# Kernel optimization log

Measured on AMD Instinct MI355X. Metric: run time of the kernel, lower is better.

The kernel has to match this reference:

```python
import jax, jax.numpy as jnp
import numpy as np

DIM = 768
N_HEADS = 12
HEAD_DIM = DIM // N_HEADS
BATCH = 2
SEQ = 4096


def setup_inputs() -> dict:
    key = jax.random.key(0)
    ks = jax.random.split(key, 9)
    s = 1.0 / np.sqrt(DIM)
    return {
        "x": jax.random.normal(ks[0], (BATCH, SEQ, DIM), dtype=jnp.float32),
        "Wq": jax.random.normal(ks[1], (DIM, DIM), dtype=jnp.float32) * s,
        "bq": jax.random.normal(ks[2], (DIM,), dtype=jnp.float32) * s,
        "Wk": jax.random.normal(ks[3], (DIM, DIM), dtype=jnp.float32) * s,
        "bk": jax.random.normal(ks[4], (DIM,), dtype=jnp.float32) * s,
        "Wv": jax.random.normal(ks[5], (DIM, DIM), dtype=jnp.float32) * s,
        "bv": jax.random.normal(ks[6], (DIM,), dtype=jnp.float32) * s,
        "Wo": jax.random.normal(ks[7], (DIM, DIM), dtype=jnp.float32) * s,
        "bo": jax.random.normal(ks[8], (DIM,), dtype=jnp.float32) * s,
    }


def reference(x, Wq, bq, Wk, bk, Wv, bv, Wo, bo):
    B, S, D = x.shape
    scale = 1.0 / np.sqrt(HEAD_DIM).astype(np.float32)
    # projections: [B,S,D] -> [B,H,S,Hd]
    def split_heads(t):
        return t.reshape(B, S, N_HEADS, HEAD_DIM).transpose(0, 2, 1, 3)
    q = split_heads(x @ Wq + bq)
    k = split_heads(x @ Wk + bk)
    v = split_heads(x @ Wv + bv)
    # full score matrix [B,H,S,S] as in the original (memory-bound)
    scores = jnp.einsum("bhqd,bhkd->bhqk", q, k) * scale
    attn = jax.nn.softmax(scores, axis=-1)
    out = jnp.einsum("bhqk,bhkd->bhqd", attn, v)
    out = out.transpose(0, 2, 1, 3).reshape(B, S, D)
    return out @ Wo + bo
```

## Files before the change

### kernel.cpp

```cpp
#include <hip/hip_runtime.h>
#include <hip/hip_bf16.h>
#include <math.h>

#define D_MODEL 768
#define NH 12
#define HD 64
#define BATCH 2
#define SEQ 4096
#define NROWS (BATCH * SEQ)

#define QSCALE 0.18033688011112042f

typedef __attribute__((ext_vector_type(8))) short short8;
typedef __attribute__((ext_vector_type(4))) short short4v;
typedef __attribute__((ext_vector_type(4))) float f32x4;
typedef __attribute__((ext_vector_type(16))) float f32x16;
typedef __attribute__((ext_vector_type(4))) unsigned int uint4v;

__device__ inline unsigned short f2bf(float f) {
    __hip_bfloat16 h = __float2bfloat16(f);
    return *reinterpret_cast<unsigned short*>(&h);
}

__device__ __forceinline__ unsigned int cvtpk_bf16(float lo, float hi) {
    unsigned int d;
    asm("v_cvt_pk_bf16_f32 %0, %1, %2" : "=v"(d) : "v"(lo), "v"(hi));
    return d;
}

__device__ __forceinline__ short8 u4_as_s8(uint4v u) {
    return *reinterpret_cast<short8*>(&u);
}

__device__ __forceinline__ void async_ld16(const unsigned short* g, unsigned short* l) {
    __builtin_amdgcn_global_load_lds(
        (const __attribute__((address_space(1))) void*)g,
        (__attribute__((address_space(3))) void*)l, 16, 0, 0);
}

__global__ __launch_bounds__(256) void convert_x_k(
    const float* __restrict__ x, unsigned short* __restrict__ xb)
{
    size_t i = ((size_t)blockIdx.x * 256 + threadIdx.x) * 8;
    float4 a = *(const float4*)(x + i);
    float4 b = *(const float4*)(x + i + 4);
    short8 o;
    o[0] = (short)f2bf(a.x); o[1] = (short)f2bf(a.y);
    o[2] = (short)f2bf(a.z); o[3] = (short)f2bf(a.w);
    o[4] = (short)f2bf(b.x); o[5] = (short)f2bf(b.y);
    o[6] = (short)f2bf(b.z); o[7] = (short)f2bf(b.w);
    *(short8*)(xb + i) = o;
}

__global__ __launch_bounds__(256) void convert_wt_k(
    const float* __restrict__ Wq, const float* __restrict__ Wk,
    const float* __restrict__ Wv, const float* __restrict__ Wo,
    unsigned short* __restrict__ wt)
{
    const float* W = (blockIdx.z == 0) ? Wq : (blockIdx.z == 1) ? Wk
                   : (blockIdx.z == 2) ? Wv : Wo;
    unsigned short* dst = wt + (size_t)blockIdx.z * D_MODEL * D_MODEL;
    __shared__ float tile[64][65];
    const int k0 = blockIdx.x * 64, n0 = blockIdx.y * 64;
    const int t = threadIdx.x;
    const int r = t >> 2, seg = t & 3;
    const float* src = W + (size_t)(k0 + r) * D_MODEL + n0 + seg * 16;
    #pragma unroll
    for (int i = 0; i < 4; ++i) {
        float4 v = *(const float4*)(src + i * 4);
        tile[r][seg * 16 + i * 4 + 0] = v.x;
        tile[r][seg * 16 + i * 4 + 1] = v.y;
        tile[r][seg * 16 + i * 4 + 2] = v.z;
        tile[r][seg * 16 + i * 4 + 3] = v.w;
    }
    __syncthreads();
    unsigned short* d = dst + (size_t)(n0 + r) * D_MODEL + k0 + seg * 16;
    short8 o0, o1;
    #pragma unroll
    for (int j = 0; j < 8; ++j) o0[j] = (short)f2bf(tile[seg * 16 + j][r]);
    #pragma unroll
    for (int j = 0; j < 8; ++j) o1[j] = (short)f2bf(tile[seg * 16 + 8 + j][r]);
    *(short8*)(d) = o0;
    *(short8*)(d + 8) = o1;
}

__global__ __launch_bounds__(256, 3) void qkv_fused_k(
    const unsigned short* __restrict__ xb,
    const unsigned short* __restrict__ wt,
    const float* __restrict__ bq, const float* __restrict__ bk,
    const float* __restrict__ bv,
    unsigned short* __restrict__ qb,
    unsigned short* __restrict__ kb,
    unsigned short* __restrict__ vtb)
{
    __shared__ unsigned short As[128][64];
    __shared__ unsigned short Bs[3][64][64];
    const int t = threadIdx.x;
    const int w = t >> 6, lane = t & 63, quad = lane >> 4, col = lane & 15;
    const int r0 = blockIdx.x * 128;
    const int c0 = blockIdx.y * 64;

    f32x4 acc[3][2][4] = {};

    for (int kk = 0; kk < D_MODEL; kk += 64) {
        __syncthreads();
        #pragma unroll
        for (int j = 0; j < 4; ++j) {
            int c = (w * 4 + j) * 64 + lane;
            async_ld16(xb + (size_t)(r0 + (c >> 3)) * D_MODEL + kk + (c & 7) * 8,
                       &As[0][0] + (size_t)c * 8);
        }
        #pragma unroll
        for (int z = 0; z < 3; ++z) {
            const unsigned short* Wt = wt + (size_t)z * D_MODEL * D_MODEL;
            #pragma unroll
            for (int j = 0; j < 2; ++j) {
                int c = (w * 2 + j) * 64 + lane;
                async_ld16(Wt + (size_t)(c0 + (c >> 3)) * D_MODEL + kk + (c & 7) * 8,
                           &Bs[z][0][0] + (size_t)c * 8);
            }
        }
        __syncthreads();
        #pragma unroll
        for (int ks = 0; ks < 2; ++ks) {
            short8 af[2];
            af[0] = *(const short8*)&As[w * 32 + col][ks * 32 + quad * 8];
            af[1] = *(const short8*)&As[w * 32 + 16 + col][ks * 32 + quad * 8];
            #pragma unroll
            for (int z = 0; z < 3; ++z) {
                short8 bf[4];
                #pragma unroll
                for (int nt = 0; nt < 4; ++nt)
                    bf[nt] = *(const short8*)&Bs[z][nt * 16 + col][ks * 32 + quad * 8];
                #pragma unroll
                for (int mt = 0; mt < 2; ++mt)
                    #pragma unroll
                    for (int nt = 0; nt < 4; ++nt)
                        acc[z][mt][nt] = __builtin_amdgcn_mfma_f32_16x16x32_bf16(
                            af[mt], bf[nt], acc[z][mt][nt], 0, 0, 0);
            }
        }
    }

    const int h = blockIdx.y;
    #pragma unroll
    for (int z = 0; z < 3; ++z) {
        const float* bias = (z == 0) ? bq : (z == 1) ? bk : bv;
        #pragma unroll
        for (int nt = 0; nt < 4; ++nt) {
            const float bv_ = bias[c0 + nt * 16 + col];
            const int hd = nt * 16 + col;
            #pragma unroll
            for (int mt = 0; mt < 2; ++mt) {
                #pragma unroll
                for (int reg = 0; reg < 4; ++reg) {
                    int r = r0 + w * 32 + mt * 16 + quad * 4 + reg;
                    int b = r >> 12, s = r & (SEQ - 1);
                    float val = acc[z][mt][nt][reg] + bv_;
                    size_t bh = (size_t)(b * NH + h);
                    size_t bhb = bh * (size_t)(SEQ * HD);
                    if (z == 0) {
                        qb[(bh * SEQ + s) * HD + hd] = f2bf(val * QSCALE);
                    } else if (z == 1) {
                        size_t idx = bhb + (size_t)(s >> 6) * 4096
                                   + (size_t)((s >> 5) & 1) * 2048
                                   + (size_t)(hd >> 4) * 512
                                   + (size_t)((hd >> 3) & 1) * 256
                                   + (size_t)(s & 31) * 8 + (hd & 7);
                        kb[idx] = f2bf(val);
                    } else {
                        size_t idx = bhb + (size_t)(s >> 6) * 4096
                                   + (size_t)(hd >> 5) * 2048
                                   + (size_t)((s >> 4) & 3) * 512
                                   + (size_t)((s >> 3) & 1) * 256
                                   + (size_t)(hd & 31) * 8 + (s & 7);
                        vtb[idx] = f2bf(val);
                    }
                }
            }
        }
    }
}

#define GEMM_STAGE(AS, BS, APTR, BPTR, KK)                                   \
    {                                                                        \
        _Pragma("unroll")                                                    \
        for (int j = 0; j < 4; ++j) {                                        \
            int c = (w * 4 + j) * 64 + lane;                                 \
            async_ld16(APTR + (size_t)(r0 + (c >> 3)) * D_MODEL + (KK) + (c & 7) * 8, \
                       &AS[0][0] + (size_t)c * 8);                           \
        }                                                                    \
        _Pragma("unroll")                                                    \
        for (int j = 0; j < 2; ++j) {                                        \
            int c = (w * 2 + j) * 64 + lane;                                 \
            async_ld16(BPTR + (size_t)(c0 + (c >> 3)) * D_MODEL + (KK) + (c & 7) * 8, \
                       &BS[0][0] + (size_t)c * 8);                           \
        }                                                                    \
    }

#define GEMM_COMPUTE(AS, BS)                                                 \
    {                                                                        \
        _Pragma("unroll")                                                    \
        for (int ks = 0; ks < 2; ++ks) {                                     \
            short8 af[2], bf[4];                                             \
            af[0] = *(const short8*)&AS[w * 32 + col][ks * 32 + quad * 8];   \
            af[1] = *(const short8*)&AS[w * 32 + 16 + col][ks * 32 + quad * 8]; \
            _Pragma("unroll")                                                \
            for (int nt = 0; nt < 4; ++nt)                                   \
                bf[nt] = *(const short8*)&BS[nt * 16 + col][ks * 32 + quad * 8]; \
            _Pragma("unroll")                                                \
            for (int mt = 0; mt < 2; ++mt)                                   \
                _Pragma("unroll")                                            \
                for (int nt = 0; nt < 4; ++nt)                               \
                    acc[mt][nt] = __builtin_amdgcn_mfma_f32_16x16x32_bf16(   \
                        af[mt], bf[nt], acc[mt][nt], 0, 0, 0);               \
        }                                                                    \
    }

__global__ __launch_bounds__(256) void out_mfma_k(
    const unsigned short* __restrict__ ab,
    const unsigned short* __restrict__ wot,
    const float* __restrict__ bo,
    float* __restrict__ out)
{
    __shared__ unsigned short As0[128][64], As1[128][64];
    __shared__ unsigned short Bs0[64][64],  Bs1[64][64];
    const int t = threadIdx.x;
    const int w = t >> 6, lane = t & 63, quad = lane >> 4, col = lane & 15;
    const int r0 = blockIdx.x * 128;
    const int c0 = blockIdx.y * 64;

    f32x4 acc[2][4] = {};

    GEMM_STAGE(As0, Bs0, ab, wot, 0);
    __syncthreads();
    #pragma unroll
    for (int kp = 0; kp < 6; ++kp) {
        GEMM_STAGE(As1, Bs1, ab, wot, kp * 128 + 64);
        GEMM_COMPUTE(As0, Bs0);
        __syncthreads();
        if (kp < 5) GEMM_STAGE(As0, Bs0, ab, wot, kp * 128 + 128);
        GEMM_COMPUTE(As1, Bs1);
        __syncthreads();
    }

    #pragma unroll
    for (int nt = 0; nt < 4; ++nt) {
        const float bv_ = bo[c0 + nt * 16 + col];
        #pragma unroll
        for (int mt = 0; mt < 2; ++mt) {
            #pragma unroll
            for (int reg = 0; reg < 4; ++reg) {
                int r = r0 + w * 32 + mt * 16 + quad * 4 + reg;
                out[(size_t)r * D_MODEL + c0 + nt * 16 + col] = acc[mt][nt][reg] + bv_;
            }
        }
    }
}

__device__ __forceinline__ void softmax_pack(
    const f32x16& s, float& lsum, short8& pf0, short8& pf1)
{
    float p[16];
    #pragma unroll
    for (int r = 0; r < 16; ++r)
        p[r] = __builtin_amdgcn_exp2f(s[r]);
    lsum += (((p[0] + p[1]) + (p[2] + p[3])) + ((p[4] + p[5]) + (p[6] + p[7])))
          + (((p[8] + p[9]) + (p[10] + p[11])) + ((p[12] + p[13]) + (p[14] + p[15])));
    unsigned int c01 = cvtpk_bf16(p[0],  p[1]);
    unsigned int c45 = cvtpk_bf16(p[4],  p[5]);
    unsigned int c23 = cvtpk_bf16(p[2],  p[3]);
    unsigned int c67 = cvtpk_bf16(p[6],  p[7]);
    unsigned int c89 = cvtpk_bf16(p[8],  p[9]);
    unsigned int cCD = cvtpk_bf16(p[12], p[13]);
    unsigned int cAB = cvtpk_bf16(p[10], p[11]);
    unsigned int cEF = cvtpk_bf16(p[14], p[15]);
    auto r0 = __builtin_amdgcn_permlane32_swap((int)c01, (int)c45, false, false);
    auto r1 = __builtin_amdgcn_permlane32_swap((int)c23, (int)c67, false, false);
    auto r2 = __builtin_amdgcn_permlane32_swap((int)c89, (int)cCD, false, false);
    auto r3 = __builtin_amdgcn_permlane32_swap((int)cAB, (int)cEF, false, false);
    uint4v u0, u1;
    u0[0] = (unsigned int)r0[0]; u0[1] = (unsigned int)r1[0];
    u0[2] = (unsigned int)r0[1]; u0[3] = (unsigned int)r1[1];
    u1[0] = (unsigned int)r2[0]; u1[1] = (unsigned int)r3[0];
    u1[2] = (unsigned int)r2[1]; u1[3] = (unsigned int)r3[1];
    pf0 = u4_as_s8(u0);
    pf1 = u4_as_s8(u1);
}

__global__ __launch_bounds__(256) void flash_mfma_k(
    const unsigned short* __restrict__ qb,
    const unsigned short* __restrict__ kb,
    const unsigned short* __restrict__ vtb,
    unsigned short* __restrict__ ab)
{
    const int t = threadIdx.x;
    const int w = t >> 6, lane = t & 63;
    const int l31 = lane & 31, hi = lane >> 5;
    const int bid = blockIdx.x;
    const int lid = (bid & 7) * 96 + (bid >> 3);
    const int q0 = (lid & 31) * 128;
    const int hb = lid >> 5;
    const int h = hb % NH, b = hb / NH;
    const size_t bh = (size_t)b * NH + h;
    const unsigned short* qg = qb + bh * SEQ * HD;
    const unsigned short* kgt = kb + bh * (size_t)(SEQ * HD);
    const unsigned short* vgt = vtb + bh * (size_t)(SEQ * HD);

    short8 qf[4];
    {
        const unsigned short* src = qg + (size_t)(q0 + w * 32 + l31) * HD + hi * 8;
        #pragma unroll
        for (int ks = 0; ks < 4; ++ks)
            qf[ks] = *(const short8*)(src + ks * 16);
    }

    f32x16 oacc[2] = {};
    float lsum = 0.f;

    for (int T = 0; T < SEQ / 64; ++T) {
        const unsigned short* kT = kgt + (size_t)T * 4096 + (size_t)lane * 8;
        const unsigned short* vT = vgt + (size_t)T * 4096 + (size_t)lane * 8;
        short8 kf0 = *(const short8*)(kT);
        short8 kf1 = *(const short8*)(kT + 512);
        short8 kf2 = *(const short8*)(kT + 1024);
        short8 kf3 = *(const short8*)(kT + 1536);
        short8 kf4 = *(const short8*)(kT + 2048);
        short8 kf5 = *(const short8*)(kT + 2560);
        short8 kf6 = *(const short8*)(kT + 3072);
        short8 kf7 = *(const short8*)(kT + 3584);

        short8 pf[4];
        {
            f32x16 s = {};
            __builtin_amdgcn_s_setprio(1);
            s = __builtin_amdgcn_mfma_f32_32x32x16_bf16(kf0, qf[0], s, 0, 0, 0);
            s = __builtin_amdgcn_mfma_f32_32x32x16_bf16(kf1, qf[1], s, 0, 0, 0);
            s = __builtin_amdgcn_mfma_f32_32x32x16_bf16(kf2, qf[2], s, 0, 0, 0);
            s = __builtin_amdgcn_mfma_f32_32x32x16_bf16(kf3, qf[3], s, 0, 0, 0);
            __builtin_amdgcn_s_setprio(0);
            softmax_pack(s, lsum, pf[0], pf[1]);
        }
        {
            f32x16 s = {};
            __builtin_amdgcn_s_setprio(1);
            s = __builtin_amdgcn_mfma_f32_32x32x16_bf16(kf4, qf[0], s, 0, 0, 0);
            s = __builtin_amdgcn_mfma_f32_32x32x16_bf16(kf5, qf[1], s, 0, 0, 0);
            s = __builtin_amdgcn_mfma_f32_32x32x16_bf16(kf6, qf[2], s, 0, 0, 0);
            s = __builtin_amdgcn_mfma_f32_32x32x16_bf16(kf7, qf[3], s, 0, 0, 0);
            __builtin_amdgcn_s_setprio(0);
            softmax_pack(s, lsum, pf[2], pf[3]);
        }

        __builtin_amdgcn_s_setprio(1);
        #pragma unroll
        for (int ks = 0; ks < 4; ++ks) {
            short8 pfk = pf[ks];
            short8 vf0 = *(const short8*)(vT + (size_t)ks * 512);
            oacc[0] = __builtin_amdgcn_mfma_f32_32x32x16_bf16(vf0, pfk, oacc[0], 0, 0, 0);
            short8 vf1 = *(const short8*)(vT + (size_t)(4 + ks) * 512);
            oacc[1] = __builtin_amdgcn_mfma_f32_32x32x16_bf16(vf1, pfk, oacc[1], 0, 0, 0);
        }
        __builtin_amdgcn_s_setprio(0);
    }

    lsum += __shfl_xor(lsum, 32);
    float inv = 1.0f / lsum;
    int s = q0 + w * 32 + l31;
    unsigned short* dst = ab + ((size_t)b * SEQ + s) * D_MODEL + h * HD;
    #pragma unroll
    for (int dt = 0; dt < 2; ++dt) {
        #pragma unroll
        for (int rq = 0; rq < 4; ++rq) {
            short4v o4;
            o4[0] = (short)f2bf(oacc[dt][rq * 4 + 0] * inv);
            o4[1] = (short)f2bf(oacc[dt][rq * 4 + 1] * inv);
            o4[2] = (short)f2bf(oacc[dt][rq * 4 + 2] * inv);
            o4[3] = (short)f2bf(oacc[dt][rq * 4 + 3] * inv);
            *(short4v*)(dst + dt * 32 + rq * 8 + hi * 4) = o4;
        }
    }
}

extern "C" void kernel_launch(void* const* d_in, const int* in_sizes, int n_in,
                              void* d_out, int out_size, void* d_ws, size_t ws_size,
                              hipStream_t stream)
{
    const float* x  = (const float*)d_in[0];
    const float* Wq = (const float*)d_in[1];
    const float* bq = (const float*)d_in[2];
    const float* Wk = (const float*)d_in[3];
    const float* bk = (const float*)d_in[4];
    const float* Wv = (const float*)d_in[5];
    const float* bv = (const float*)d_in[6];
    const float* Wo = (const float*)d_in[7];
    const float* bo = (const float*)d_in[8];
    float* out = (float*)d_out;

    const size_t n_x  = (size_t)NROWS * D_MODEL;
    const size_t n_w  = (size_t)D_MODEL * D_MODEL;
    unsigned short* xb  = (unsigned short*)d_ws;
    unsigned short* wt  = xb + n_x;
    unsigned short* qb  = wt + 4 * n_w;
    unsigned short* kb  = qb + n_x;
    unsigned short* vtb = kb + n_x;
    unsigned short* ab  = vtb + n_x;
    const size_t need = ((size_t)5 * n_x + 4 * n_w) * sizeof(unsigned short);
    if (ws_size < need) return;

    convert_x_k<<<dim3((int)(n_x / 2048)), 256, 0, stream>>>(x, xb);
    convert_wt_k<<<dim3(12, 12, 4), 256, 0, stream>>>(Wq, Wk, Wv, Wo, wt);
    qkv_fused_k<<<dim3(NROWS / 128, D_MODEL / 64), 256, 0, stream>>>(
        xb, wt, bq, bk, bv, qb, kb, vtb);
    flash_mfma_k<<<dim3(SEQ / 128 * NH * BATCH), 256, 0, stream>>>(
        qb, kb, vtb, ab);
    out_mfma_k<<<dim3(NROWS / 128, D_MODEL / 64), 256, 0, stream>>>(
        ab, wt + 3 * n_w, bo, out);
}
```

Measured before the change: 288.3 us.

## Split KV range across two wave groups per block and reduce via LDS

Doubles the flash attention block to 512 threads. Each half of the waves processes half of the key/value tiles for the same 128 query rows. The second half writes its partial output accumulators and row sums to shared memory, and the first half combines them and writes the normalized bf16 result. This is meant to add parallelism and latency hiding per query tile, at the cost of extra LDS traffic, a block barrier and higher per-block resource use.

```diff
diff --git a/kernel.cpp b/kernel.cpp
--- a/kernel.cpp
+++ b/kernel.cpp
@@ -288,14 +288,18 @@
     pf1 = u4_as_s8(u1);
 }
 
-__global__ __launch_bounds__(256) void flash_mfma_k(
+__global__ __launch_bounds__(512) void flash_mfma_k(
     const unsigned short* __restrict__ qb,
     const unsigned short* __restrict__ kb,
     const unsigned short* __restrict__ vtb,
     unsigned short* __restrict__ ab)
 {
+    __shared__ float Osh[4][32][68];
+    __shared__ float Lsh[4][32];
+
     const int t = threadIdx.x;
     const int w = t >> 6, lane = t & 63;
+    const int wsub = w & 3, half = w >> 2;
     const int l31 = lane & 31, hi = lane >> 5;
     const int bid = blockIdx.x;
     const int lid = (bid & 7) * 96 + (bid >> 3);
@@ -309,7 +313,7 @@
 
     short8 qf[4];
     {
-        const unsigned short* src = qg + (size_t)(q0 + w * 32 + l31) * HD + hi * 8;
+        const unsigned short* src = qg + (size_t)(q0 + wsub * 32 + l31) * HD + hi * 8;
         #pragma unroll
         for (int ks = 0; ks < 4; ++ks)
             qf[ks] = *(const short8*)(src + ks * 16);
@@ -318,7 +322,8 @@
     f32x16 oacc[2] = {};
     float lsum = 0.f;
 
-    for (int T = 0; T < SEQ / 64; ++T) {
+    const int T0 = half * 32;
+    for (int T = T0; T < T0 + 32; ++T) {
         const unsigned short* kT = kgt + (size_t)T * 4096 + (size_t)lane * 8;
         const unsigned short* vT = vgt + (size_t)T * 4096 + (size_t)lane * 8;
         short8 kf0 = *(const short8*)(kT);
@@ -365,19 +370,38 @@
     }
 
     lsum += __shfl_xor(lsum, 32);
-    float inv = 1.0f / lsum;
-    int s = q0 + w * 32 + l31;
-    unsigned short* dst = ab + ((size_t)b * SEQ + s) * D_MODEL + h * HD;
-    #pragma unroll
-    for (int dt = 0; dt < 2; ++dt) {
-        #pragma unroll
-        for (int rq = 0; rq < 4; ++rq) {
-            short4v o4;
-            o4[0] = (short)f2bf(oacc[dt][rq * 4 + 0] * inv);
-            o4[1] = (short)f2bf(oacc[dt][rq * 4 + 1] * inv);
-            o4[2] = (short)f2bf(oacc[dt][rq * 4 + 2] * inv);
-            o4[3] = (short)f2bf(oacc[dt][rq * 4 + 3] * inv);
-            *(short4v*)(dst + dt * 32 + rq * 8 + hi * 4) = o4;
+    if (half == 1) {
+        #pragma unroll
+        for (int dt = 0; dt < 2; ++dt) {
+            #pragma unroll
+            for (int rq = 0; rq < 4; ++rq) {
+                f32x4 v;
+                v[0] = oacc[dt][rq * 4 + 0];
+                v[1] = oacc[dt][rq * 4 + 1];
+                v[2] = oacc[dt][rq * 4 + 2];
+                v[3] = oacc[dt][rq * 4 + 3];
+                *(f32x4*)&Osh[wsub][l31][dt * 32 + rq * 8 + hi * 4] = v;
+            }
+        }
+        if (hi == 0) Lsh[wsub][l31] = lsum;
+    }
+    __syncthreads();
+    if (half == 0) {
+        float inv = 1.0f / (lsum + Lsh[wsub][l31]);
+        int s = q0 + wsub * 32 + l31;
+        unsigned short* dst = ab + ((size_t)b * SEQ + s) * D_MODEL + h * HD;
+        #pragma unroll
+        for (int dt = 0; dt < 2; ++dt) {
+            #pragma unroll
+            for (int rq = 0; rq < 4; ++rq) {
+                f32x4 o = *(const f32x4*)&Osh[wsub][l31][dt * 32 + rq * 8 + hi * 4];
+                short4v o4;
+                o4[0] = (short)f2bf((oacc[dt][rq * 4 + 0] + o[0]) * inv);
+                o4[1] = (short)f2bf((oacc[dt][rq * 4 + 1] + o[1]) * inv);
+                o4[2] = (short)f2bf((oacc[dt][rq * 4 + 2] + o[2]) * inv);
+                o4[3] = (short)f2bf((oacc[dt][rq * 4 + 3] + o[3]) * inv);
+                *(short4v*)(dst + dt * 32 + rq * 8 + hi * 4) = o4;
+            }
         }
     }
 }
@@ -412,7 +436,7 @@
     convert_wt_k<<<dim3(12, 12, 4), 256, 0, stream>>>(Wq, Wk, Wv, Wo, wt);
     qkv_fused_k<<<dim3(NROWS / 128, D_MODEL / 64), 256, 0, stream>>>(
         xb, wt, bq, bk, bv, qb, kb, vtb);
-    flash_mfma_k<<<dim3(SEQ / 128 * NH * BATCH), 256, 0, stream>>>(
+    flash_mfma_k<<<dim3(SEQ / 128 * NH * BATCH), 512, 0, stream>>>(
         qb, kb, vtb, ab);
     out_mfma_k<<<dim3(NROWS / 128, D_MODEL / 64), 256, 0, stream>>>(
         ab, wt + 3 * n_w, bo, out);
```

Result: no change. 287.0 us (-0.5%).

## Stage K/V tiles through double-buffered LDS and compute row sums with MFMA

Applied to the files above, without the earlier changes.

K and V^T tiles are now loaded asynchronously into double-buffered shared memory and shared by all four waves, replacing the per-wave direct global loads, with the next tile prefetched while the current one is processed. The softmax row-sum is moved from VALU adds into an extra MFMA against a ones vector. The aim is to cut redundant global traffic and load latency and to offload VALU work. The cost is a block barrier every iteration, an extra MFMA per k-step, and the row sum now accumulating bf16-rounded probabilities.

```diff
diff --git a/kernel.cpp b/kernel.cpp
--- a/kernel.cpp
+++ b/kernel.cpp
@@ -259,14 +259,12 @@
 }
 
 __device__ __forceinline__ void softmax_pack(
-    const f32x16& s, float& lsum, short8& pf0, short8& pf1)
+    const f32x16& s, short8& pf0, short8& pf1)
 {
     float p[16];
     #pragma unroll
     for (int r = 0; r < 16; ++r)
         p[r] = __builtin_amdgcn_exp2f(s[r]);
-    lsum += (((p[0] + p[1]) + (p[2] + p[3])) + ((p[4] + p[5]) + (p[6] + p[7])))
-          + (((p[8] + p[9]) + (p[10] + p[11])) + ((p[12] + p[13]) + (p[14] + p[15])));
     unsigned int c01 = cvtpk_bf16(p[0],  p[1]);
     unsigned int c45 = cvtpk_bf16(p[4],  p[5]);
     unsigned int c23 = cvtpk_bf16(p[2],  p[3]);
@@ -294,6 +292,9 @@
     const unsigned short* __restrict__ vtb,
     unsigned short* __restrict__ ab)
 {
+    __shared__ unsigned short Ks[2][4096];
+    __shared__ unsigned short Vts[2][4096];
+
     const int t = threadIdx.x;
     const int w = t >> 6, lane = t & 63;
     const int l31 = lane & 31, hi = lane >> 5;
@@ -315,57 +316,65 @@
             qf[ks] = *(const short8*)(src + ks * 16);
     }
 
+    short8 ones;
+    #pragma unroll
+    for (int j = 0; j < 8; ++j) ones[j] = (short)0x3F80;
+
     f32x16 oacc[2] = {};
-    float lsum = 0.f;
-
+    f32x16 lacc = {};
+
+    #pragma unroll
+    for (int j = 0; j < 2; ++j) {
+        int c = w * 2 + j;
+        async_ld16(kgt + (size_t)c * 512 + (size_t)lane * 8, &Ks[0][c * 512]);
+        async_ld16(vgt + (size_t)c * 512 + (size_t)lane * 8, &Vts[0][c * 512]);
+    }
+
+    int buf = 0;
     for (int T = 0; T < SEQ / 64; ++T) {
-        const unsigned short* kT = kgt + (size_t)T * 4096 + (size_t)lane * 8;
-        const unsigned short* vT = vgt + (size_t)T * 4096 + (size_t)lane * 8;
-        short8 kf0 = *(const short8*)(kT);
-        short8 kf1 = *(const short8*)(kT + 512);
-        short8 kf2 = *(const short8*)(kT + 1024);
-        short8 kf3 = *(const short8*)(kT + 1536);
-        short8 kf4 = *(const short8*)(kT + 2048);
-        short8 kf5 = *(const short8*)(kT + 2560);
-        short8 kf6 = *(const short8*)(kT + 3072);
-        short8 kf7 = *(const short8*)(kT + 3584);
+        __syncthreads();
+        if (T + 1 < SEQ / 64) {
+            const size_t tb = (size_t)(T + 1) * 4096;
+            int nb = buf ^ 1;
+            #pragma unroll
+            for (int j = 0; j < 2; ++j) {
+                int c = w * 2 + j;
+                async_ld16(kgt + tb + (size_t)c * 512 + (size_t)lane * 8,
+                           &Ks[nb][c * 512]);
+                async_ld16(vgt + tb + (size_t)c * 512 + (size_t)lane * 8,
+                           &Vts[nb][c * 512]);
+            }
+        }
 
         short8 pf[4];
-        {
+        #pragma unroll
+        for (int kti = 0; kti < 2; ++kti) {
             f32x16 s = {};
             __builtin_amdgcn_s_setprio(1);
-            s = __builtin_amdgcn_mfma_f32_32x32x16_bf16(kf0, qf[0], s, 0, 0, 0);
-            s = __builtin_amdgcn_mfma_f32_32x32x16_bf16(kf1, qf[1], s, 0, 0, 0);
-            s = __builtin_amdgcn_mfma_f32_32x32x16_bf16(kf2, qf[2], s, 0, 0, 0);
-            s = __builtin_amdgcn_mfma_f32_32x32x16_bf16(kf3, qf[3], s, 0, 0, 0);
+            #pragma unroll
+            for (int ks = 0; ks < 4; ++ks) {
+                short8 kf = *(const short8*)&Ks[buf][(kti * 4 + ks) * 512 + lane * 8];
+                s = __builtin_amdgcn_mfma_f32_32x32x16_bf16(kf, qf[ks], s, 0, 0, 0);
+            }
             __builtin_amdgcn_s_setprio(0);
-            softmax_pack(s, lsum, pf[0], pf[1]);
-        }
-        {
-            f32x16 s = {};
-            __builtin_amdgcn_s_setprio(1);
-            s = __builtin_amdgcn_mfma_f32_32x32x16_bf16(kf4, qf[0], s, 0, 0, 0);
-            s = __builtin_amdgcn_mfma_f32_32x32x16_bf16(kf5, qf[1], s, 0, 0, 0);
-            s = __builtin_amdgcn_mfma_f32_32x32x16_bf16(kf6, qf[2], s, 0, 0, 0);
-            s = __builtin_amdgcn_mfma_f32_32x32x16_bf16(kf7, qf[3], s, 0, 0, 0);
-            __builtin_amdgcn_s_setprio(0);
-            softmax_pack(s, lsum, pf[2], pf[3]);
+            softmax_pack(s, pf[kti * 2 + 0], pf[kti * 2 + 1]);
         }
 
         __builtin_amdgcn_s_setprio(1);
         #pragma unroll
         for (int ks = 0; ks < 4; ++ks) {
             short8 pfk = pf[ks];
-            short8 vf0 = *(const short8*)(vT + (size_t)ks * 512);
+            short8 vf0 = *(const short8*)&Vts[buf][ks * 512 + lane * 8];
             oacc[0] = __builtin_amdgcn_mfma_f32_32x32x16_bf16(vf0, pfk, oacc[0], 0, 0, 0);
-            short8 vf1 = *(const short8*)(vT + (size_t)(4 + ks) * 512);
+            short8 vf1 = *(const short8*)&Vts[buf][(4 + ks) * 512 + lane * 8];
             oacc[1] = __builtin_amdgcn_mfma_f32_32x32x16_bf16(vf1, pfk, oacc[1], 0, 0, 0);
+            lacc = __builtin_amdgcn_mfma_f32_32x32x16_bf16(ones, pfk, lacc, 0, 0, 0);
         }
         __builtin_amdgcn_s_setprio(0);
-    }
-
-    lsum += __shfl_xor(lsum, 32);
-    float inv = 1.0f / lsum;
+        buf ^= 1;
+    }
+
+    float inv = 1.0f / lacc[0];
     int s = q0 + w * 32 + l31;
     unsigned short* dst = ab + ((size_t)b * SEQ + s) * D_MODEL + h * HD;
     #pragma unroll
```

Measured after the change: 279.9 us. 2.9% less time.

## Stage K/V tiles through triple-buffered LDS with async loads in flash kernel

Applied to the files above, without the earlier changes.

Replaces per-wave direct global loads of K and V^T tiles with a cooperative, triple-buffered LDS pipeline. Asynchronous 16-byte global-to-LDS loads prefetch two tiles ahead, and each iteration ends with a vmcnt wait and a block barrier. Each wave now issues only a quarter of the global loads instead of every wave loading the full tile redundantly, and load latency overlaps with the MFMA and softmax work. In exchange it adds 48KB of LDS per block, which may reduce occupancy, plus a barrier every iteration and LDS read traffic.

```diff
diff --git a/kernel.cpp b/kernel.cpp
--- a/kernel.cpp
+++ b/kernel.cpp
@@ -294,6 +294,9 @@
     const unsigned short* __restrict__ vtb,
     unsigned short* __restrict__ ab)
 {
+    __shared__ unsigned short Ks[3][4096];
+    __shared__ unsigned short Vts[3][4096];
+
     const int t = threadIdx.x;
     const int w = t >> 6, lane = t & 63;
     const int l31 = lane & 31, hi = lane >> 5;
@@ -314,55 +317,73 @@
         for (int ks = 0; ks < 4; ++ks)
             qf[ks] = *(const short8*)(src + ks * 16);
     }
+    asm volatile("s_waitcnt vmcnt(0)" ::: "memory");
 
     f32x16 oacc[2] = {};
     float lsum = 0.f;
 
-    for (int T = 0; T < SEQ / 64; ++T) {
-        const unsigned short* kT = kgt + (size_t)T * 4096 + (size_t)lane * 8;
-        const unsigned short* vT = vgt + (size_t)T * 4096 + (size_t)lane * 8;
-        short8 kf0 = *(const short8*)(kT);
-        short8 kf1 = *(const short8*)(kT + 512);
-        short8 kf2 = *(const short8*)(kT + 1024);
-        short8 kf3 = *(const short8*)(kT + 1536);
-        short8 kf4 = *(const short8*)(kT + 2048);
-        short8 kf5 = *(const short8*)(kT + 2560);
-        short8 kf6 = *(const short8*)(kT + 3072);
-        short8 kf7 = *(const short8*)(kT + 3584);
-
-        short8 pf[4];
-        {
-            f32x16 s = {};
-            __builtin_amdgcn_s_setprio(1);
-            s = __builtin_amdgcn_mfma_f32_32x32x16_bf16(kf0, qf[0], s, 0, 0, 0);
-            s = __builtin_amdgcn_mfma_f32_32x32x16_bf16(kf1, qf[1], s, 0, 0, 0);
-            s = __builtin_amdgcn_mfma_f32_32x32x16_bf16(kf2, qf[2], s, 0, 0, 0);
-            s = __builtin_amdgcn_mfma_f32_32x32x16_bf16(kf3, qf[3], s, 0, 0, 0);
-            __builtin_amdgcn_s_setprio(0);
-            softmax_pack(s, lsum, pf[0], pf[1]);
-        }
-        {
-            f32x16 s = {};
-            __builtin_amdgcn_s_setprio(1);
-            s = __builtin_amdgcn_mfma_f32_32x32x16_bf16(kf4, qf[0], s, 0, 0, 0);
-            s = __builtin_amdgcn_mfma_f32_32x32x16_bf16(kf5, qf[1], s, 0, 0, 0);
-            s = __builtin_amdgcn_mfma_f32_32x32x16_bf16(kf6, qf[2], s, 0, 0, 0);
-            s = __builtin_amdgcn_mfma_f32_32x32x16_bf16(kf7, qf[3], s, 0, 0, 0);
-            __builtin_amdgcn_s_setprio(0);
-            softmax_pack(s, lsum, pf[2], pf[3]);
-        }
-
-        __builtin_amdgcn_s_setprio(1);
-        #pragma unroll
-        for (int ks = 0; ks < 4; ++ks) {
-            short8 pfk = pf[ks];
-            short8 vf0 = *(const short8*)(vT + (size_t)ks * 512);
-            oacc[0] = __builtin_amdgcn_mfma_f32_32x32x16_bf16(vf0, pfk, oacc[0], 0, 0, 0);
-            short8 vf1 = *(const short8*)(vT + (size_t)(4 + ks) * 512);
-            oacc[1] = __builtin_amdgcn_mfma_f32_32x32x16_bf16(vf1, pfk, oacc[1], 0, 0, 0);
-        }
-        __builtin_amdgcn_s_setprio(0);
-    }
+#define FLASH_STAGE(SLOT, T)                                                  \
+    {                                                                         \
+        const size_t tb = (size_t)(T) * 4096;                                 \
+        _Pragma("unroll")                                                     \
+        for (int j = 0; j < 2; ++j) {                                         \
+            int c = w * 2 + j;                                                \
+            async_ld16(kgt + tb + (size_t)c * 512 + (size_t)lane * 8,         \
+                       &Ks[SLOT][c * 512]);                                   \
+            async_ld16(vgt + tb + (size_t)c * 512 + (size_t)lane * 8,         \
+                       &Vts[SLOT][c * 512]);                                  \
+        }                                                                     \
+    }
+
+#define FLASH_COMPUTE(SLOT)                                                   \
+    {                                                                         \
+        short8 pf[4];                                                         \
+        _Pragma("unroll")                                                     \
+        for (int kti = 0; kti < 2; ++kti) {                                   \
+            f32x16 s = {};                                                    \
+            __builtin_amdgcn_s_setprio(1);                                    \
+            _Pragma("unroll")                                                 \
+            for (int ks = 0; ks < 4; ++ks) {                                  \
+                short8 kf = *(const short8*)&Ks[SLOT][(kti * 4 + ks) * 512 + lane * 8]; \
+                s = __builtin_amdgcn_mfma_f32_32x32x16_bf16(kf, qf[ks], s, 0, 0, 0);    \
+            }                                                                 \
+            __builtin_amdgcn_s_setprio(0);                                    \
+            softmax_pack(s, lsum, pf[kti * 2 + 0], pf[kti * 2 + 1]);          \
+        }                                                                     \
+        __builtin_amdgcn_s_setprio(1);                                        \
+        _Pragma("unroll")                                                     \
+        for (int ks = 0; ks < 4; ++ks) {                                      \
+            short8 pfk = pf[ks];                                              \
+            short8 vf0 = *(const short8*)&Vts[SLOT][ks * 512 + lane * 8];     \
+            oacc[0] = __builtin_amdgcn_mfma_f32_32x32x16_bf16(vf0, pfk, oacc[0], 0, 0, 0); \
+            short8 vf1 = *(const short8*)&Vts[SLOT][(4 + ks) * 512 + lane * 8];            \
+            oacc[1] = __builtin_amdgcn_mfma_f32_32x32x16_bf16(vf1, pfk, oacc[1], 0, 0, 0); \
+        }                                                                     \
+        __builtin_amdgcn_s_setprio(0);                                        \
+    }
+
+    const int NT = SEQ / 64;
+    FLASH_STAGE(0, 0);
+    FLASH_STAGE(1, 1);
+
+    int cs = 0;
+    int ss = 2;
+    for (int T = 0; T < NT - 1; ++T) {
+        asm volatile("s_waitcnt vmcnt(4)" ::: "memory");
+        __builtin_amdgcn_s_barrier();
+        __builtin_amdgcn_sched_barrier(0);
+        if (T + 2 < NT) FLASH_STAGE(ss, T + 2);
+        FLASH_COMPUTE(cs);
+        cs = (cs == 2) ? 0 : cs + 1;
+        ss = (ss == 2) ? 0 : ss + 1;
+    }
+    asm volatile("s_waitcnt vmcnt(0)" ::: "memory");
+    __builtin_amdgcn_s_barrier();
+    __builtin_amdgcn_sched_barrier(0);
+    FLASH_COMPUTE(cs);
+
+#undef FLASH_STAGE
+#undef FLASH_COMPUTE
 
     lsum += __shfl_xor(lsum, 32);
     float inv = 1.0f / lsum;
```

Measured after the change: 285.8 us. About the same (-0.9%).
